# Kernel optimization log

Hardware: AMD Instinct MI355X
Metric: run time of the kernel (lower is better)

## Reference

```python
import jax, jax.numpy as jnp
from jax import lax
import numpy as np

# --- constants from Vessel_Enhance_Block defaults ---
MIN_MAX = (0.0, 500.0)
ALPHA, BETA, GAMMA = 0.5, 1.0, 5.0          # frangi_param[0:3]
SIGMAS = tuple(np.arange(1.0, 2.5, 0.3).tolist())  # [1.0,1.3,1.6,1.9,2.2]
FRANGI_TH = 0.2
TH_LO, TH_HI = 0.1, 0.5                     # th_param
MIN_SIZE = 200


def _gauss_kernel1d(sigma, order):
    """scipy.ndimage-style Gaussian derivative kernel (truncate=4)."""
    radius = int(4.0 * sigma + 0.5)
    x = np.arange(-radius, radius + 1)
    phi = np.exp(-0.5 * x ** 2 / sigma ** 2)
    phi /= phi.sum()
    if order == 0:
        return phi
    exps = np.arange(order + 1)
    q = np.zeros(order + 1); q[0] = 1.0
    D = np.diag(exps[1:], 1)
    P = np.diag(np.full(order, -1.0 / sigma ** 2), -1)
    for _ in range(order):
        q = (D + P) @ q
    return (x[:, None].astype(float) ** exps @ q) * phi


def _corr1d(x, k, axis):
    """scipy gaussian_filter1d == correlate with k[::-1] == convolve with k.
    lax.conv is a correlation, so pass k reversed. mode='reflect' (symmetric)."""
    x = jnp.moveaxis(x, axis, -1)
    shp = x.shape
    r = (k.shape[0] - 1) // 2
    xp = jnp.pad(x.reshape(-1, 1, shp[-1]), ((0, 0), (0, 0), (r, r)), mode='symmetric')
    kern = jnp.asarray(k[::-1].copy(), x.dtype).reshape(1, 1, -1)
    y = lax.conv_general_dilated(xp, kern, (1,), 'VALID')
    return jnp.moveaxis(y.reshape(shp), -1, axis)


def _frangi(img):
    """2D Frangi vesselness, black_ridges=False, img: [B,H,W]."""
    img = -img  # black_ridges=False -> negate image
    out = jnp.zeros_like(img)
    for sigma in SIGMAS:
        k0 = _gauss_kernel1d(sigma, 0)
        k1 = _gauss_kernel1d(sigma, 1)
        k2 = _gauss_kernel1d(sigma, 2)
        s2 = jnp.asarray(sigma ** 2, img.dtype)  # scale normalization
        Hrr = _corr1d(_corr1d(img, k2, 1), k0, 2) * s2
        Hrc = _corr1d(_corr1d(img, k1, 1), k1, 2) * s2
        Hcc = _corr1d(_corr1d(img, k0, 1), k2, 2) * s2
        mid = 0.5 * (Hrr + Hcc)
        disc = jnp.sqrt(jnp.square(0.5 * (Hrr - Hcc)) + jnp.square(Hrc))
        e_hi, e_lo = mid + disc, mid - disc
        small = jnp.abs(e_hi) <= jnp.abs(e_lo)  # sort eigenvalues by magnitude
        lam1 = jnp.where(small, e_hi, e_lo)     # |lam1| <= |lam2|
        lam2 = jnp.where(small, e_lo, e_hi)
        lam2c = jnp.maximum(lam2, 1e-10)
        r_b2 = jnp.square(lam1 / lam2c)                       # blobness^2
        s_sq = jnp.square(lam1) + jnp.square(lam2)            # structuredness^2
        vals = jnp.exp(-r_b2 / (2.0 * BETA ** 2)) * (1.0 - jnp.exp(-s_sq / (2.0 * GAMMA ** 2)))
        out = jnp.maximum(out, vals)
    return out


def _remove_small(mask, min_size):
    """remove_small_objects(connectivity=2): drop 8-connected components < min_size."""
    H, W = mask.shape
    BIG = H * W
    idx = jnp.arange(BIG, dtype=jnp.int32).reshape(H, W)
    lab0 = jnp.where(mask, idx, BIG)

    def nmin(lab):  # min over 8-neighborhood, restricted to mask
        p = jnp.pad(lab, 1, constant_values=BIG)
        m = lab
        for di in (0, 1, 2):
            for dj in (0, 1, 2):
                if di == 1 and dj == 1:
                    continue
                m = jnp.minimum(m, lax.dynamic_slice(p, (di, dj), (H, W)))
        return jnp.where(mask, m, BIG)

    def jump(lab):  # pointer jumping: lab <- lab[lab]
        flat = lab.reshape(-1)
        ext = jnp.concatenate([flat, jnp.array([BIG], flat.dtype)])
        return ext[flat].reshape(H, W)

    def body(st):
        lab, _ = st
        return jump(jump(nmin(lab))), lab

    def cond(st):
        lab, prev = st
        return jnp.any(lab != prev)

    lab, _ = lax.while_loop(cond, body, (nmin(lab0), lab0))
    sizes = jnp.zeros(BIG + 1, jnp.int32).at[lab.reshape(-1)].add(mask.reshape(-1).astype(jnp.int32))
    return (sizes[lab] >= min_size) & mask


def setup_inputs() -> dict:
    key = jax.random.key(0)
    image = jax.random.uniform(key, (16, 1, 512, 512), dtype=jnp.float32)
    return {"image": image}


def reference(image):
    x = image[:, 0]                                   # [B,H,W]
    th_mask = (x >= TH_LO) & (x <= TH_HI)             # get_th
    scaled = x * (MIN_MAX[1] - MIN_MAX[0]) + MIN_MAX[0]
    fr = _frangi(scaled)
    fmask = th_mask & (fr >= FRANGI_TH)               # th & frangi masks
    out = jax.vmap(lambda m: _remove_small(m, MIN_SIZE))(fmask)
    return out[:, None]                               # [B,1,H,W] bool
```

## Files before the change

kernel.cpp:

```cpp
#include <hip/hip_runtime.h>
#include <math.h>
#include <string.h>

#define IMG_H   512
#define IMG_W   512
#define NPIX    (IMG_H*IMG_W)
#define NIMG    16
#define NSIG    5
#define MIN_SZ  200
#define SSTR    60
#define SROWS   52
#define TSTR    68
#define KVL     20
#define KHL     24
#define NBLK    65536

typedef float f4 __attribute__((ext_vector_type(4)));

struct KTab {
  float kv[NSIG][3][KVL];
  float kh[NSIG][3][KHL];
  float s2[NSIG];
};

template<int SIG, int RAD, int MLO, int GH, int LP4, int L4P>
__device__ __forceinline__ void do_sigma(const float* __restrict__ sIn,
                                         float* __restrict__ t0,
                                         float* __restrict__ t1,
                                         float* __restrict__ t2,
                                         const KTab& kt, int tid, float* fr)
{
  if (tid < 32*GH) {
    int r0 = tid & 31;
    int h  = tid >> 5;
    int a  = (r0 + 9 - RAD)*SSTR + 4*(MLO + 2*h);
    f4 A0={0,0,0,0}, A1={0,0,0,0}, A2={0,0,0,0};
    f4 B0={0,0,0,0}, B1={0,0,0,0}, B2={0,0,0,0};
#pragma unroll 1
    for (int jj = 0; jj < LP4/4; ++jj) {
      f4 w0 = *(const f4*)&kt.kv[SIG][0][4*jj];
      f4 w1 = *(const f4*)&kt.kv[SIG][1][4*jj];
      f4 w2 = *(const f4*)&kt.kv[SIG][2][4*jj];
#pragma unroll
      for (int u = 0; u < 4; ++u) {
        f4 xA = *(const f4*)(sIn + a);
        f4 xB = *(const f4*)(sIn + a + 4);
        a += SSTR;
        A0 += xA*w0[u]; A1 += xA*w1[u]; A2 += xA*w2[u];
        B0 += xB*w0[u]; B1 += xB*w1[u]; B2 += xB*w2[u];
      }
    }
    int tb = r0*TSTR + 4*(MLO + 2*h);
    *(f4*)(t0 + tb)     = A0; *(f4*)(t1 + tb)     = A1; *(f4*)(t2 + tb)     = A2;
    *(f4*)(t0 + tb + 4) = B0; *(f4*)(t1 + tb + 4) = B1; *(f4*)(t2 + tb + 4) = B2;
  }
  __syncthreads();

  {
    int r  = tid >> 3;
    int c0 = (tid & 7) * 4;
    int wa = r*TSTR + 4*MLO + c0;
    f4 P0 = *(const f4*)(t0 + wa);
    f4 P1 = *(const f4*)(t1 + wa);
    f4 P2 = *(const f4*)(t2 + wa);
    f4 Q0 = *(const f4*)(t0 + wa + 4);
    f4 Q1 = *(const f4*)(t1 + wa + 4);
    f4 Q2 = *(const f4*)(t2 + wa + 4);
    wa += 8;
    f4 hrr={0,0,0,0}, hrc={0,0,0,0}, hcc={0,0,0,0};
#pragma unroll 1
    for (int aa = 0; aa < L4P/8; ++aa) {
      {
        f4 w0 = *(const f4*)&kt.kh[SIG][0][8*aa];
        f4 w1 = *(const f4*)&kt.kh[SIG][1][8*aa];
        f4 w2 = *(const f4*)&kt.kh[SIG][2][8*aa];
#pragma unroll
        for (int b = 0; b < 4; ++b)
#pragma unroll
          for (int k = 0; k < 4; ++k) {
            int e = b + k;
            float x2 = (e < 4) ? P2[e] : Q2[e-4];
            float x1 = (e < 4) ? P1[e] : Q1[e-4];
            float x0 = (e < 4) ? P0[e] : Q0[e-4];
            hrr[k] += x2 * w0[b];
            hrc[k] += x1 * w1[b];
            hcc[k] += x0 * w2[b];
          }
        P0 = *(const f4*)(t0 + wa);
        P1 = *(const f4*)(t1 + wa);
        P2 = *(const f4*)(t2 + wa);
      }
      {
        f4 w0 = *(const f4*)&kt.kh[SIG][0][8*aa+4];
        f4 w1 = *(const f4*)&kt.kh[SIG][1][8*aa+4];
        f4 w2 = *(const f4*)&kt.kh[SIG][2][8*aa+4];
#pragma unroll
        for (int b = 0; b < 4; ++b)
#pragma unroll
          for (int k = 0; k < 4; ++k) {
            int e = b + k;
            float x2 = (e < 4) ? Q2[e] : P2[e-4];
            float x1 = (e < 4) ? Q1[e] : P1[e-4];
            float x0 = (e < 4) ? Q0[e] : P0[e-4];
            hrr[k] += x2 * w0[b];
            hrc[k] += x1 * w1[b];
            hcc[k] += x0 * w2[b];
          }
        Q0 = *(const f4*)(t0 + wa + 4);
        Q1 = *(const f4*)(t1 + wa + 4);
        Q2 = *(const f4*)(t2 + wa + 4);
      }
      wa += 8;
    }
    float s2v = kt.s2[SIG];
#pragma unroll
    for (int k = 0; k < 4; ++k) {
      float Hrr = hrr[k]*s2v, Hrc = hrc[k]*s2v, Hcc = hcc[k]*s2v;
      float mid  = 0.5f*(Hrr + Hcc);
      float dif  = 0.5f*(Hrr - Hcc);
      float disc = sqrtf(dif*dif + Hrc*Hrc);
      float ehi  = mid + disc;
      float elo  = mid - disc;
      bool  sm   = fabsf(ehi) <= fabsf(elo);
      float lam1 = sm ? ehi : elo;
      float lam2 = sm ? elo : ehi;
      float lam2c = fmaxf(lam2, 1e-10f);
      float q    = lam1 / lam2c;
      float rb2  = q*q;
      float ssq  = lam1*lam1 + lam2*lam2;
      float v    = __expf((-rb2)/2.0f) * (1.0f - __expf((-ssq)/50.0f));
      fr[k] = fmaxf(fr[k], v);
    }
  }
  __syncthreads();
}

__global__ __launch_bounds__(256)
void frangi_label_kernel(const float* __restrict__ img,
                         int* __restrict__ labels,
                         int* __restrict__ parent,
                         int* __restrict__ bsizes,
                         KTab kt)
{
  __shared__ float sIn[SROWS*SSTR];
  __shared__ float t0[32*TSTR];
  __shared__ float t1[32*TSTR];
  __shared__ float t2[32*TSTR];

  const int tid    = threadIdx.x;
  const int imgIdx = blockIdx.y;
  const int tIdx   = blockIdx.x;
  const int tr0    = (tIdx >> 4) * 32;
  const int tc0    = (tIdx & 15) * 32;
  const float* __restrict__ im = img + (size_t)imgIdx * NPIX;

  for (int idx = tid; idx < SROWS*64; idx += 256) {
    int r  = idx >> 6;
    int cs = idx & 63;
    if (cs < SSTR) {
      float v = 0.0f;
      if (r < 50 && cs >= 3 && cs < 53) {
        int gr = tr0 + r - 9;
        int gc = tc0 + cs - 12;
        gr = (gr < 0) ? (-1 - gr) : ((gr >= IMG_H) ? (2*IMG_H - 1 - gr) : gr);
        gc = (gc < 0) ? (-1 - gc) : ((gc >= IMG_W) ? (2*IMG_W - 1 - gc) : gc);
        v = -(im[gr*IMG_W + gc] * 500.0f);
      }
      sIn[r*SSTR + cs] = v;
    }
  }
  __syncthreads();

  float fr[4] = {0.0f, 0.0f, 0.0f, 0.0f};
  do_sigma<0,  4,  2,  6, 12, 16>(sIn, t0, t1, t2, kt, tid, fr);
  do_sigma<1,  5,  1,  6, 12, 16>(sIn, t0, t1, t2, kt, tid, fr);
  do_sigma<2,  6,  1,  6, 16, 16>(sIn, t0, t1, t2, kt, tid, fr);
  do_sigma<3,  8,  1,  7, 20, 24>(sIn, t0, t1, t2, kt, tid, fr);
  do_sigma<4,  9,  0,  7, 20, 24>(sIn, t0, t1, t2, kt, tid, fr);

  const int r  = tid >> 3;
  const int c0 = (tid & 7) * 4;
  const int gr = tr0 + r;
  const size_t imgBase = (size_t)imgIdx * NPIX;
#pragma unroll
  for (int k = 0; k < 4; ++k) {
    int p = gr*IMG_W + tc0 + c0 + k;
    float x = im[p];
    bool m = (x >= 0.1f) && (x <= 0.5f) && (fr[k] >= 0.2f);
    labels[imgBase + p] = m ? p : -1;
  }
  {
    int blk = (tr0/2 + (tid >> 4))*256 + (tc0/2 + (tid & 15));
    int o   = (imgIdx << 16) + blk;
    parent[o] = blk;
    bsizes[o] = 0;
  }
}

__device__ __forceinline__ int ldA(const int* p) {
  return __hip_atomic_load(p, __ATOMIC_RELAXED, __HIP_MEMORY_SCOPE_AGENT);
}
__device__ __forceinline__ int rootOf(const int* L, int x) {
  int pa = ldA(&L[x]);
  while (pa != x) { int g = ldA(&L[pa]); x = pa; pa = g; }
  return x;
}
__device__ __forceinline__ void unite(int* P, int a, int b) {
  while (true) {
    a = rootOf(P, a);
    b = rootOf(P, b);
    if (a == b) return;
    int hi = a > b ? a : b;
    int lo = a ^ b ^ hi;
    int old = atomicCAS(&P[hi], hi, lo);
    if (old == hi) return;
    a = old; b = lo;
  }
}

__global__ __launch_bounds__(256)
void merge_kernel(const int* __restrict__ labels, int* __restrict__ parent)
{
  int gid = blockIdx.x*256 + threadIdx.x;
  int img = gid >> 16;
  int blk = gid & (NBLK - 1);
  int BR = blk >> 8, BC = blk & 255;
  const int* L = labels + ((size_t)img << 18);
  int p = BR*1024 + BC*2;
  int2 t = *(const int2*)(L + p);
  int2 bm = *(const int2*)(L + p + 512);
  bool f00 = t.x >= 0, f01 = t.y >= 0, f10 = bm.x >= 0, f11 = bm.y >= 0;
  if (!(f00 | f01 | f10 | f11)) return;
  int* P = parent + (img << 16);
  if (BC > 0 && (f00 | f10) && (L[p-1] >= 0 || L[p+511] >= 0))
    unite(P, blk, blk-1);
  if (BR > 0) {
    int2 n = *(const int2*)(L + p - 512);
    if ((f00 | f01) && (n.x >= 0 || n.y >= 0)) unite(P, blk, blk-256);
    if (BC > 0   && f00 && L[p-513] >= 0)      unite(P, blk, blk-257);
    if (BC < 255 && f01 && L[p-510] >= 0)      unite(P, blk, blk-255);
  }
}

__global__ __launch_bounds__(256)
void compress_count_kernel(const int* __restrict__ labels,
                           int* __restrict__ parent, int* __restrict__ bsizes)
{
  int gid = blockIdx.x*256 + threadIdx.x;
  int img = gid >> 16;
  int blk = gid & (NBLK - 1);
  int BR = blk >> 8, BC = blk & 255;
  const int* L = labels + ((size_t)img << 18);
  int p = BR*1024 + BC*2;
  int2 t = *(const int2*)(L + p);
  int2 bm = *(const int2*)(L + p + 512);
  int cnt = (t.x >= 0) + (t.y >= 0) + (bm.x >= 0) + (bm.y >= 0);
  int* P = parent + (img << 16);
  int rt = -1;
  if (cnt) {
    rt = rootOf(P, blk);
    __hip_atomic_store(&P[blk], rt, __ATOMIC_RELAXED, __HIP_MEMORY_SCOPE_AGENT);
  }
  int lane = threadIdx.x & 63;
  int val  = cnt;
  int prt  = __shfl_up(rt, 1);
  int fseg = (lane == 0 || prt != rt) ? 1 : 0;
#pragma unroll
  for (int d = 1; d < 64; d <<= 1) {
    int v2  = __shfl_up(val, d);
    int fg2 = __shfl_up(fseg, d);
    if (lane >= d && !fseg) { val += v2; fseg |= fg2; }
  }
  int nrt = __shfl_down(rt, 1);
  bool tail = (lane == 63) || (nrt != rt);
  if (tail && rt >= 0)
    atomicAdd(&bsizes[(img << 16) + rt], val);
}

__global__ __launch_bounds__(256)
void output_kernel(const int* __restrict__ labels, const int* __restrict__ parent,
                   const int* __restrict__ bsizes, float* __restrict__ out)
{
  int qid = blockIdx.x*256 + threadIdx.x;
  int img = qid >> 16;
  int p0  = (qid & 65535) << 2;
  const int* L = labels + ((size_t)img << 18);
  int4 l4 = *(const int4*)(L + p0);
  int r = p0 >> 9, c = p0 & 511;
  int blk0 = (r >> 1)*256 + (c >> 1);
  const int* P = parent + (img << 16);
  const int* S = bsizes + (img << 16);
  int2 pp = *(const int2*)(P + blk0);
  float4 o;
  o.x = (l4.x >= 0 && S[pp.x] >= MIN_SZ) ? 1.0f : 0.0f;
  o.y = (l4.y >= 0 && S[pp.x] >= MIN_SZ) ? 1.0f : 0.0f;
  o.z = (l4.z >= 0 && S[pp.y] >= MIN_SZ) ? 1.0f : 0.0f;
  o.w = (l4.w >= 0 && S[pp.y] >= MIN_SZ) ? 1.0f : 0.0f;
  *(float4*)(out + ((size_t)qid << 2)) = o;
}

static void gauss1d(double sigma, int order, int rad, float* out)
{
  int L = 2*rad + 1;
  double phi[24];
  double s = 0.0;
  for (int i = 0; i < L; ++i) {
    double x = (double)(i - rad);
    phi[i] = exp(-0.5*x*x/(sigma*sigma));
    s += phi[i];
  }
  for (int i = 0; i < L; ++i) phi[i] /= s;
  if (order == 0) {
    for (int i = 0; i < L; ++i) out[i] = (float)phi[i];
    return;
  }
  double q[3] = {1.0, 0.0, 0.0};
  for (int it = 0; it < order; ++it) {
    double nq[3] = {0.0, 0.0, 0.0};
    for (int i = 0; i <= order; ++i) {
      double v = 0.0;
      if (i+1 <= order) v += (double)(i+1) * q[i+1];
      if (i-1 >= 0)     v += (-1.0/(sigma*sigma)) * q[i-1];
      nq[i] = v;
    }
    q[0] = nq[0]; q[1] = nq[1]; q[2] = nq[2];
  }
  for (int i = 0; i < L; ++i) {
    double x = (double)(i - rad);
    double poly = q[0];
    double xp = x;
    for (int e = 1; e <= order; ++e) { poly += xp*q[e]; xp *= x; }
    out[i] = (float)(poly*phi[i]);
  }
}

extern "C" void kernel_launch(void* const* d_in, const int* in_sizes, int n_in,
                              void* d_out, int out_size, void* d_ws, size_t ws_size,
                              hipStream_t stream)
{
  (void)in_sizes; (void)n_in; (void)out_size; (void)ws_size;
  const float* img = (const float*)d_in[0];
  float* out = (float*)d_out;
  int* labels = (int*)d_ws;
  int* parent = labels + (size_t)NIMG * NPIX;
  int* bsizes = parent + (size_t)NIMG * NBLK;

  KTab kt;
  memset(&kt, 0, sizeof(kt));
  for (int s = 0; s < NSIG; ++s) {
    double sigma = 1.0 + 0.3 * (double)s;
    int rad = (int)(4.0 * sigma + 0.5);
    int L   = 2*rad + 1;
    int dlt = (12 - rad) & 3;
    kt.s2[s] = (float)(sigma * sigma);
    float k[3][24];
    for (int o = 0; o < 3; ++o) gauss1d(sigma, o, rad, k[o]);
    for (int o = 0; o < 3; ++o) {
      for (int j = 0; j < L; ++j)
        kt.kv[s][o][j] = k[o][L-1-j];
      for (int jp = 0; jp < KHL; ++jp)
        kt.kh[s][o][jp] = (jp >= dlt && jp - dlt < L) ? k[o][L-1-(jp-dlt)] : 0.0f;
    }
  }

  dim3 gridF(NPIX / (32*32), NIMG);
  frangi_label_kernel<<<gridF, 256, 0, stream>>>(img, labels, parent, bsizes, kt);

  int bblocks = (NIMG * NBLK) / 256;
  merge_kernel         <<<bblocks, 256, 0, stream>>>(labels, parent);
  compress_count_kernel<<<bblocks, 256, 0, stream>>>(labels, parent, bsizes);
  output_kernel        <<<bblocks, 256, 0, stream>>>(labels, parent, bsizes, out);
}
```

Measured before the change: 196.8 us.

## Widen Frangi tiles to 32x64 with 512-thread blocks to cut halo overhead

Each Frangi block now covers a 32x64 output tile with 512 threads instead of 32x32 with 256, so the fixed vertical and horizontal halo is shared across twice as many outputs. The shared-memory strides, kernel tap alignment offset and column-group counts are retuned to match. Partial last column groups for the larger sigmas are handled with a flag, and an odd trailing horizontal tap group is added. The larger tiles mean fewer blocks and more LDS per block, which may reduce occupancy and parallelism.

```diff
diff --git a/kernel.cpp b/kernel.cpp
--- a/kernel.cpp
+++ b/kernel.cpp
@@ -8,9 +8,10 @@
 #define NIMG    16
 #define NSIG    5
 #define MIN_SZ  200
-#define SSTR    60
+#define SSTR    84
 #define SROWS   52
-#define TSTR    68
+#define TSTR    92
+#define TSZ     (32*TSTR)
 #define KVL     20
 #define KHL     24
 #define NBLK    65536
@@ -23,7 +24,7 @@
   float s2[NSIG];
 };
 
-template<int SIG, int RAD, int MLO, int GH, int LP4, int L4P>
+template<int SIG, int RAD, int MLO, int GH, bool HL, int LP4, int L4P>
 __device__ __forceinline__ void do_sigma(const float* __restrict__ sIn,
                                          float* __restrict__ t0,
                                          float* __restrict__ t1,
@@ -33,7 +34,9 @@
   if (tid < 32*GH) {
     int r0 = tid & 31;
     int h  = tid >> 5;
+    bool doB = !HL || (h < GH-1);
     int a  = (r0 + 9 - RAD)*SSTR + 4*(MLO + 2*h);
+    int bo = doB ? 4 : 0;
     f4 A0={0,0,0,0}, A1={0,0,0,0}, A2={0,0,0,0};
     f4 B0={0,0,0,0}, B1={0,0,0,0}, B2={0,0,0,0};
 #pragma unroll 1
@@ -44,7 +47,7 @@
 #pragma unroll
       for (int u = 0; u < 4; ++u) {
         f4 xA = *(const f4*)(sIn + a);
-        f4 xB = *(const f4*)(sIn + a + 4);
+        f4 xB = *(const f4*)(sIn + a + bo);
         a += SSTR;
         A0 += xA*w0[u]; A1 += xA*w1[u]; A2 += xA*w2[u];
         B0 += xB*w0[u]; B1 += xB*w1[u]; B2 += xB*w2[u];
@@ -52,13 +55,15 @@
     }
     int tb = r0*TSTR + 4*(MLO + 2*h);
     *(f4*)(t0 + tb)     = A0; *(f4*)(t1 + tb)     = A1; *(f4*)(t2 + tb)     = A2;
-    *(f4*)(t0 + tb + 4) = B0; *(f4*)(t1 + tb + 4) = B1; *(f4*)(t2 + tb + 4) = B2;
+    if (doB) {
+      *(f4*)(t0 + tb + 4) = B0; *(f4*)(t1 + tb + 4) = B1; *(f4*)(t2 + tb + 4) = B2;
+    }
   }
   __syncthreads();
 
   {
-    int r  = tid >> 3;
-    int c0 = (tid & 7) * 4;
+    int r  = tid >> 4;
+    int c0 = (tid & 15) * 4;
     int wa = r*TSTR + 4*MLO + c0;
     f4 P0 = *(const f4*)(t0 + wa);
     f4 P1 = *(const f4*)(t1 + wa);
@@ -112,6 +117,23 @@
       }
       wa += 8;
     }
+    if constexpr (((L4P/4) & 1) != 0) {
+      f4 w0 = *(const f4*)&kt.kh[SIG][0][L4P-4];
+      f4 w1 = *(const f4*)&kt.kh[SIG][1][L4P-4];
+      f4 w2 = *(const f4*)&kt.kh[SIG][2][L4P-4];
+#pragma unroll
+      for (int b = 0; b < 4; ++b)
+#pragma unroll
+        for (int k = 0; k < 4; ++k) {
+          int e = b + k;
+          float x2 = (e < 4) ? P2[e] : Q2[e-4];
+          float x1 = (e < 4) ? P1[e] : Q1[e-4];
+          float x0 = (e < 4) ? P0[e] : Q0[e-4];
+          hrr[k] += x2 * w0[b];
+          hrc[k] += x1 * w1[b];
+          hcc[k] += x0 * w2[b];
+        }
+    }
     float s2v = kt.s2[SIG];
 #pragma unroll
     for (int k = 0; k < 4; ++k) {
@@ -135,51 +157,51 @@
   __syncthreads();
 }
 
-__global__ __launch_bounds__(256)
+__global__ __launch_bounds__(512)
 void frangi_label_kernel(const float* __restrict__ img,
                          int* __restrict__ labels,
                          int* __restrict__ parent,
                          int* __restrict__ bsizes,
                          KTab kt)
 {
-  __shared__ float sIn[SROWS*SSTR];
-  __shared__ float t0[32*TSTR];
-  __shared__ float t1[32*TSTR];
-  __shared__ float t2[32*TSTR];
+  __shared__ float lds[3*TSZ + SROWS*SSTR];
+  float* t0  = lds;
+  float* t1  = lds + TSZ;
+  float* t2  = lds + 2*TSZ;
+  float* sIn = lds + 3*TSZ;
 
   const int tid    = threadIdx.x;
   const int imgIdx = blockIdx.y;
   const int tIdx   = blockIdx.x;
-  const int tr0    = (tIdx >> 4) * 32;
-  const int tc0    = (tIdx & 15) * 32;
+  const int tr0    = (tIdx >> 3) * 32;
+  const int tc0    = (tIdx & 7) * 64;
   const float* __restrict__ im = img + (size_t)imgIdx * NPIX;
 
-  for (int idx = tid; idx < SROWS*64; idx += 256) {
-    int r  = idx >> 6;
-    int cs = idx & 63;
-    if (cs < SSTR) {
-      float v = 0.0f;
-      if (r < 50 && cs >= 3 && cs < 53) {
-        int gr = tr0 + r - 9;
-        int gc = tc0 + cs - 12;
-        gr = (gr < 0) ? (-1 - gr) : ((gr >= IMG_H) ? (2*IMG_H - 1 - gr) : gr);
-        gc = (gc < 0) ? (-1 - gc) : ((gc >= IMG_W) ? (2*IMG_W - 1 - gc) : gc);
-        v = -(im[gr*IMG_W + gc] * 500.0f);
-      }
-      sIn[r*SSTR + cs] = v;
-    }
+  for (int i = tid; i < 3*TSZ; i += 512) lds[i] = 0.0f;
+  for (int idx = tid; idx < SROWS*SSTR; idx += 512) {
+    int r  = idx / SSTR;
+    int cs = idx - r*SSTR;
+    float v = 0.0f;
+    if (r < 50 && cs >= 2) {
+      int gr = tr0 + r - 9;
+      int gc = tc0 + cs - 11;
+      gr = (gr < 0) ? (-1 - gr) : ((gr >= IMG_H) ? (2*IMG_H - 1 - gr) : gr);
+      gc = (gc < 0) ? (-1 - gc) : ((gc >= IMG_W) ? (2*IMG_W - 1 - gc) : gc);
+      v = -(im[gr*IMG_W + gc] * 500.0f);
+    }
+    sIn[idx] = v;
   }
   __syncthreads();
 
   float fr[4] = {0.0f, 0.0f, 0.0f, 0.0f};
-  do_sigma<0,  4,  2,  6, 12, 16>(sIn, t0, t1, t2, kt, tid, fr);
-  do_sigma<1,  5,  1,  6, 12, 16>(sIn, t0, t1, t2, kt, tid, fr);
-  do_sigma<2,  6,  1,  6, 16, 16>(sIn, t0, t1, t2, kt, tid, fr);
-  do_sigma<3,  8,  1,  7, 20, 24>(sIn, t0, t1, t2, kt, tid, fr);
-  do_sigma<4,  9,  0,  7, 20, 24>(sIn, t0, t1, t2, kt, tid, fr);
-
-  const int r  = tid >> 3;
-  const int c0 = (tid & 7) * 4;
+  do_sigma<0,  4,  1, 10, false, 12, 12>(sIn, t0, t1, t2, kt, tid, fr);
+  do_sigma<1,  5,  1, 10, false, 12, 16>(sIn, t0, t1, t2, kt, tid, fr);
+  do_sigma<2,  6,  1, 10, false, 16, 16>(sIn, t0, t1, t2, kt, tid, fr);
+  do_sigma<3,  8,  0, 11, true,  20, 20>(sIn, t0, t1, t2, kt, tid, fr);
+  do_sigma<4,  9,  0, 11, true,  20, 24>(sIn, t0, t1, t2, kt, tid, fr);
+
+  const int r  = tid >> 4;
+  const int c0 = (tid & 15) * 4;
   const int gr = tr0 + r;
   const size_t imgBase = (size_t)imgIdx * NPIX;
 #pragma unroll
@@ -190,7 +212,7 @@
     labels[imgBase + p] = m ? p : -1;
   }
   {
-    int blk = (tr0/2 + (tid >> 4))*256 + (tc0/2 + (tid & 15));
+    int blk = (tr0/2 + (tid >> 5))*256 + (tc0/2 + (tid & 31));
     int o   = (imgIdx << 16) + blk;
     parent[o] = blk;
     bsizes[o] = 0;
@@ -351,7 +373,7 @@
     double sigma = 1.0 + 0.3 * (double)s;
     int rad = (int)(4.0 * sigma + 0.5);
     int L   = 2*rad + 1;
-    int dlt = (12 - rad) & 3;
+    int dlt = (11 - rad) & 3;
     kt.s2[s] = (float)(sigma * sigma);
     float k[3][24];
     for (int o = 0; o < 3; ++o) gauss1d(sigma, o, rad, k[o]);
@@ -363,8 +385,8 @@
     }
   }
 
-  dim3 gridF(NPIX / (32*32), NIMG);
-  frangi_label_kernel<<<gridF, 256, 0, stream>>>(img, labels, parent, bsizes, kt);
+  dim3 gridF(128, NIMG);
+  frangi_label_kernel<<<gridF, 512, 0, stream>>>(img, labels, parent, bsizes, kt);
 
   int bblocks = (NIMG * NBLK) / 256;
   merge_kernel         <<<bblocks, 256, 0, stream>>>(labels, parent);
```

Result: slower. 234.4 us (+19.1%).
